# Optimization experiments

Hardware: AMD Instinct MI355X
Metric: run time of the kernel (lower is better)

## Reference

```python
import jax, jax.numpy as jnp
import numpy as np

K = 16  # knn_k
LN_EPS = 1e-5


def _layernorm(x, g, b):
    mu = jnp.mean(x, axis=-1, keepdims=True)
    var = jnp.var(x, axis=-1, keepdims=True)
    return (x - mu) * jax.lax.rsqrt(var + LN_EPS) * g + b


def _mlp_block(x, W1, b1, g, be, W2, b2):
    # Linear -> LayerNorm -> GELU -> Linear (MLPBlock)
    h = x @ W1 + b1
    h = jax.nn.gelu(_layernorm(h, g, be))
    return h @ W2 + b2


def _knn(v):
    # v: [N,3] -> indices of K nearest neighbors [N,K] (self included, as in knn search)
    sq = jnp.sum(v * v, axis=-1)                       # [N]
    d = sq[:, None] + sq[None, :] - 2.0 * (v @ v.T)    # [N,N] squared dists
    return jax.lax.top_k(-d, K)[1]                     # [N,K]


def setup_inputs() -> dict:
    key = jax.random.key(0)
    ks = jax.random.split(key, 8)
    B, N, C_IN, C_OUT, HID = 2, 8192, 32, 64, 128
    E_IN = C_IN + C_IN + 3  # 67
    s = 0.02
    return {
        "vertices": jax.random.normal(ks[0], (B, N, 3), jnp.float32),
        "features": jax.random.normal(ks[1], (B, N, C_IN), jnp.float32),
        "W1": jax.random.normal(ks[2], (E_IN, HID), jnp.float32) * s,
        "b1": jnp.zeros((HID,), jnp.float32),
        "g1": jnp.ones((HID,), jnp.float32),
        "be1": jnp.zeros((HID,), jnp.float32),
        "W2": jax.random.normal(ks[3], (HID, C_OUT), jnp.float32) * s,
        "b2": jnp.zeros((C_OUT,), jnp.float32),
        "Wo1": jax.random.normal(ks[4], (C_OUT, HID), jnp.float32) * s,
        "bo1": jnp.zeros((HID,), jnp.float32),
        "go": jnp.ones((HID,), jnp.float32),
        "beo": jnp.zeros((HID,), jnp.float32),
        "Wo2": jax.random.normal(ks[5], (HID, C_OUT), jnp.float32) * s,
        "bo2": jnp.zeros((C_OUT,), jnp.float32),
    }


def reference(vertices, features, W1, b1, g1, be1, W2, b2,
              Wo1, bo1, go, beo, Wo2, bo2):
    # out_point_feature_type == 'same': output points == input points
    idx = jax.vmap(_knn)(vertices)                                   # [B,N,K]
    gather = jax.vmap(lambda a, i: jnp.take(a, i, axis=0))
    neigh_feat = gather(features, idx)                               # [B,N,K,C]
    neigh_vert = gather(vertices, idx)                               # [B,N,K,3]
    self_feat = jnp.broadcast_to(features[:, :, None, :], neigh_feat.shape)
    rel_pos = neigh_vert - vertices[:, :, None, :]                   # [B,N,K,3]
    edge = jnp.concatenate([neigh_feat, self_feat, rel_pos], axis=-1)  # [B,N,K,2C+3]
    edge = _mlp_block(edge, W1, b1, g1, be1, W2, b2)                 # [B,N,K,C_out]
    out = jnp.mean(edge, axis=2)                                     # 'mean' reduction over K neighbors
    out = _mlp_block(out, Wo1, bo1, go, beo, Wo2, bo2)               # [B,N,C_out]
    return out
```

## Files before the change

### kernel.cpp

```cpp
#include <hip/hip_runtime.h>
#include <hip/hip_bf16.h>
#include <math.h>

#define BATCH 2
#define NPTS  8192
#define CIN   32
#define HID   128
#define COUT  64
#define EIN   67
#define KNN   16

#define TILE  1024
#define CAP   128
#define KMARGIN 1e-3f

typedef unsigned short u16;
typedef unsigned long long u64;
typedef __attribute__((ext_vector_type(8))) short bf16x8;
typedef __attribute__((ext_vector_type(4))) float f32x4;

#if defined(__has_builtin)
#if __has_builtin(__builtin_amdgcn_rcpf)
#define USE_RCPF 1
#endif
#endif

__device__ __forceinline__ u16 f2b(float f) {
    unsigned u = __float_as_uint(f);
    return (u16)((u + 0x7FFFu + ((u >> 16) & 1u)) >> 16);
}
__device__ __forceinline__ unsigned pk2(float a, float b) {
    return (unsigned)f2b(a) | ((unsigned)f2b(b) << 16);
}
__device__ __forceinline__ float gelu_t(float x) {
    float u = 1.5957691216057308f * (x + 0.044715f * x * x * x);
    float ex = __expf(u);
#ifdef USE_RCPF
    return x * ex * __builtin_amdgcn_rcpf(ex + 1.0f);
#else
    return x * ex / (ex + 1.0f);
#endif
}

__global__ void prep_kernel(const float* __restrict__ verts, float4* __restrict__ pv) {
    int i = blockIdx.x * blockDim.x + threadIdx.x;
    if (i >= BATCH * NPTS) return;
    float x = verts[3 * i], y = verts[3 * i + 1], z = verts[3 * i + 2];
    float sq = __fadd_rn(__fadd_rn(__fmul_rn(x, x), __fmul_rn(y, y)), __fmul_rn(z, z));
    pv[i] = make_float4(x, y, z, sq);
}

__global__ __launch_bounds__(256, 4) void knn7_kernel(const float4* __restrict__ pv,
                                                      int* __restrict__ nbr_out_rows) {
    __shared__ float4 minv4[4][64];
    __shared__ float  bufD[4][4][CAP];
    __shared__ int    bufJ[4][4][CAP];

    const int tid = threadIdx.x, lane = tid & 63, wv = tid >> 6;
    const int pt0 = (blockIdx.x * 4 + wv) * 4;
    const int b = pt0 >> 13, i0 = pt0 & (NPTS - 1);
    const float4* P = pv + (size_t)b * NPTS;

    float4 sp[4];
    float ax[4], ay[4], az[4];
#pragma unroll
    for (int p = 0; p < 4; ++p) {
        sp[p] = P[i0 + p];
        ax[p] = -2.0f * sp[p].x; ay[p] = -2.0f * sp[p].y; az[p] = -2.0f * sp[p].z;
    }

    float mn[4] = {INFINITY, INFINITY, INFINITY, INFINITY};
    for (int t = 0; t < 16; ++t) {
        float4 c0 = P[t * 256 + lane];
        float4 c1 = P[t * 256 + 64 + lane];
        float4 c2 = P[t * 256 + 128 + lane];
        float4 c3 = P[t * 256 + 192 + lane];
#pragma unroll
        for (int p = 0; p < 4; ++p) {
            float f0 = __fmaf_rn(ax[p], c0.x, __fmaf_rn(ay[p], c0.y, __fmaf_rn(az[p], c0.z, c0.w)));
            float f1 = __fmaf_rn(ax[p], c1.x, __fmaf_rn(ay[p], c1.y, __fmaf_rn(az[p], c1.z, c1.w)));
            float f2 = __fmaf_rn(ax[p], c2.x, __fmaf_rn(ay[p], c2.y, __fmaf_rn(az[p], c2.z, c2.w)));
            float f3 = __fmaf_rn(ax[p], c3.x, __fmaf_rn(ay[p], c3.y, __fmaf_rn(az[p], c3.z, c3.w)));
            mn[p] = fminf(fminf(fminf(mn[p], f0), fminf(f1, f2)), f3);
        }
    }

    minv4[wv][lane] = make_float4(mn[0], mn[1], mn[2], mn[3]);
    int rk[4] = {0, 0, 0, 0};
    for (int mm = 0; mm < 64; ++mm) {
        float4 v = minv4[wv][mm];
        rk[0] += (v.x < mn[0]) || (v.x == mn[0] && mm < lane);
        rk[1] += (v.y < mn[1]) || (v.y == mn[1] && mm < lane);
        rk[2] += (v.z < mn[2]) || (v.z == mn[2] && mm < lane);
        rk[3] += (v.w < mn[3]) || (v.w == mn[3] && mm < lane);
    }
    float tau[4];
#pragma unroll
    for (int p = 0; p < 4; ++p) {
        u64 bal = __ballot(rk[p] == 15);
        int srcl = __ffsll(bal) - 1;
        tau[p] = __shfl(mn[p], srcl, 64) + KMARGIN;
    }

    int base[4] = {0, 0, 0, 0};
    for (int t = 0; t < 32; ++t) {
        float4 c[4];
#pragma unroll
        for (int k = 0; k < 4; ++k) c[k] = P[t * 256 + k * 64 + lane];
        bool pr[4][4];
        bool anyl = false;
#pragma unroll
        for (int k = 0; k < 4; ++k)
#pragma unroll
            for (int p = 0; p < 4; ++p) {
                float f = __fmaf_rn(ax[p], c[k].x,
                          __fmaf_rn(ay[p], c[k].y,
                          __fmaf_rn(az[p], c[k].z, c[k].w)));
                pr[k][p] = (f <= tau[p]);
                anyl |= pr[k][p];
            }
        if (__ballot(anyl) == 0ull) continue;
#pragma unroll
        for (int k = 0; k < 4; ++k) {
            u64 anyk = __ballot(pr[k][0] | pr[k][1] | pr[k][2] | pr[k][3]);
            if (anyk == 0ull) continue;
            int j = t * 256 + k * 64 + lane;
#pragma unroll
            for (int p = 0; p < 4; ++p) {
                u64 mk = __ballot(pr[k][p]);
                if (mk != 0ull) {
                    if (pr[k][p]) {
                        int pos = base[p] + (int)__popcll(mk & ((1ull << lane) - 1ull));
                        if (pos < CAP) bufJ[wv][p][pos] = j;
                    }
                    base[p] += (int)__popcll(mk);
                }
            }
        }
    }

#pragma unroll
    for (int p = 0; p < 4; ++p) {
        int ns = base[p]; ns = (ns > CAP) ? CAP : ns;
        float dloc[2]; int jloc[2];
#pragma unroll
        for (int slot = 0; slot < 2; ++slot) {
            int sidx = slot * 64 + lane;
            bool act = sidx < ns;
            int js = act ? bufJ[wv][p][sidx] : 0;
            float4 cc = P[js];
            float dot = __fmul_rn(sp[p].x, cc.x);
            dot = __fmaf_rn(sp[p].y, cc.y, dot);
            dot = __fmaf_rn(sp[p].z, cc.z, dot);
            float d = __fsub_rn(__fadd_rn(sp[p].w, cc.w), __fmul_rn(2.0f, dot));
            if (act) bufD[wv][p][sidx] = d;
            dloc[slot] = d; jloc[slot] = js;
        }
        int r0 = 0, r1 = 0;
        for (int mm = 0; mm < ns; ++mm) {
            float dm = bufD[wv][p][mm]; int jm = bufJ[wv][p][mm];
            r0 += (dm < dloc[0]) || (dm == dloc[0] && jm < jloc[0]);
            r1 += (dm < dloc[1]) || (dm == dloc[1] && jm < jloc[1]);
        }
        if (lane < ns && r0 < KNN)
            nbr_out_rows[(size_t)(pt0 + p) * 64 + r0] = jloc[0];
        if (64 + lane < ns && r1 < KNN)
            nbr_out_rows[(size_t)(pt0 + p) * 64 + r1] = jloc[1];
    }
}

__global__ __launch_bounds__(256) void knn_kernel(const float* __restrict__ verts,
                                                  int* nbr_out_rows) {
    __shared__ float4 tilebuf[TILE];
    __shared__ float  bufD[4][CAP];
    __shared__ int    bufJ[4][CAP];

    const int tid = threadIdx.x, lane = tid & 63, wv = tid >> 6;
    const int pt = blockIdx.x * 4 + wv;
    const int b = pt >> 13, i = pt & (NPTS - 1);
    const float* vb = verts + (size_t)b * NPTS * 3;

    const float xi = vb[3 * i], yi = vb[3 * i + 1], zi = vb[3 * i + 2];
    const float sqi = __fadd_rn(__fadd_rn(__fmul_rn(xi, xi), __fmul_rn(yi, yi)),
                                __fmul_rn(zi, zi));

    float m_d = INFINITY;
    for (int t = 0; t < NPTS / TILE; ++t) {
        __syncthreads();
        for (int s = 0; s < TILE / 256; ++s) {
            int p = t * TILE + s * 256 + tid;
            float px = vb[3 * p], py = vb[3 * p + 1], pz = vb[3 * p + 2];
            float sq = __fadd_rn(__fadd_rn(__fmul_rn(px, px), __fmul_rn(py, py)),
                                 __fmul_rn(pz, pz));
            tilebuf[s * 256 + tid] = make_float4(px, py, pz, sq);
        }
        __syncthreads();
        for (int it = 0; it < TILE / 64; ++it) {
            float4 c = tilebuf[it * 64 + lane];
            float dot = __fmul_rn(xi, c.x);
            dot = __fmaf_rn(yi, c.y, dot);
            dot = __fmaf_rn(zi, c.z, dot);
            float d = __fsub_rn(__fadd_rn(sqi, c.w), __fmul_rn(2.0f, dot));
            m_d = fminf(m_d, d);
        }
    }
    __shared__ float minv[4][64];
    minv[wv][lane] = m_d;
    __syncthreads();
    int rnk = 0;
    for (int mm = 0; mm < 64; ++mm) {
        float vm = minv[wv][mm];
        rnk += (vm < m_d) || (vm == m_d && mm < lane);
    }
    u64 bal = __ballot(rnk == 15);
    float tau = __shfl(m_d, __ffsll(bal) - 1, 64);

    int base = 0;
    for (int t = 0; t < NPTS / TILE; ++t) {
        __syncthreads();
        for (int s = 0; s < TILE / 256; ++s) {
            int p = t * TILE + s * 256 + tid;
            float px = vb[3 * p], py = vb[3 * p + 1], pz = vb[3 * p + 2];
            float sq = __fadd_rn(__fadd_rn(__fmul_rn(px, px), __fmul_rn(py, py)),
                                 __fmul_rn(pz, pz));
            tilebuf[s * 256 + tid] = make_float4(px, py, pz, sq);
        }
        __syncthreads();
        for (int it = 0; it < TILE / 64; ++it) {
            int jl = it * 64 + lane;
            float4 c = tilebuf[jl];
            float dot = __fmul_rn(xi, c.x);
            dot = __fmaf_rn(yi, c.y, dot);
            dot = __fmaf_rn(zi, c.z, dot);
            float d = __fsub_rn(__fadd_rn(sqi, c.w), __fmul_rn(2.0f, dot));
            bool pred = (d <= tau);
            u64 mask = __ballot(pred);
            if (pred) {
                int pos = base + (int)__popcll(mask & ((1ull << lane) - 1ull));
                if (pos < CAP) { bufD[wv][pos] = d; bufJ[wv][pos] = t * TILE + jl; }
            }
            base += (int)__popcll(mask);
        }
    }
    int ns = (base > CAP) ? CAP : base;
    __syncthreads();
#pragma unroll
    for (int slot = 0; slot < 2; ++slot) {
        int sidx = slot * 64 + lane;
        if (sidx < ns) {
            float ds = bufD[wv][sidx];
            int   js = bufJ[wv][sidx];
            int rank = 0;
            for (int mm = 0; mm < ns; ++mm) {
                float dm = bufD[wv][mm];
                int   jm = bufJ[wv][mm];
                rank += (dm < ds) || (dm == ds && jm < js);
            }
            if (rank < KNN) nbr_out_rows[(size_t)pt * 64 + rank] = js;
        }
    }
}

__global__ __launch_bounds__(256, 2) void edge4_kernel(
    const float* __restrict__ verts, const float* __restrict__ feats,
    const float* __restrict__ W1, const float* __restrict__ b1,
    const float* __restrict__ g1, const float* __restrict__ be1,
    const float* __restrict__ W2, const float* __restrict__ b2,
    const float* __restrict__ Wo1, const float* __restrict__ bo1,
    const float* __restrict__ go_, const float* __restrict__ beo,
    const float* __restrict__ Wo2, const float* __restrict__ bo2,
    float* out)
{
    __shared__ u16 EPw[4][4][64][8];
    __shared__ u16 W1F[3][8][64][8];
    __shared__ float b1s[HID], g1s[HID], be1s[HID];
    __shared__ float b2s[COUT];
    __shared__ float meansh[16][68];

    const int tid  = threadIdx.x;
    const int lane = tid & 63, wv = tid >> 6;
    const int quad = lane >> 4, n16 = lane & 15;

    for (int s = tid; s < 3 * 8 * 64; s += 256) {
        int kt = s >> 9, nt = (s >> 6) & 7, ln = s & 63;
        int q = ln >> 4, nn = ln & 15;
        int col = nt * 16 + nn;
        union { bf16x8 v; unsigned u[4]; } pk;
#pragma unroll
        for (int jj = 0; jj < 4; ++jj) {
            int k0 = kt * 32 + q * 8 + jj * 2;
            float a  = (k0     < EIN) ? W1[(size_t)k0 * HID + col]       : 0.0f;
            float bq = (k0 + 1 < EIN) ? W1[(size_t)(k0 + 1) * HID + col] : 0.0f;
            pk.u[jj] = pk2(a, bq);
        }
        *(bf16x8*)&W1F[kt][nt][ln][0] = pk.v;
    }
    if (tid < HID) { b1s[tid] = b1[tid]; g1s[tid] = g1[tid]; be1s[tid] = be1[tid]; }
    if (tid < COUT) b2s[tid] = b2[tid];

    bf16x8 w2r[4][4];
#pragma unroll
    for (int kt2 = 0; kt2 < 4; ++kt2)
#pragma unroll
        for (int nt2 = 0; nt2 < 4; ++nt2) {
            union { bf16x8 v; unsigned u[4]; } pk;
#pragma unroll
            for (int jj = 0; jj < 4; ++jj) {
                int k0 = kt2 * 32 + quad * 8 + jj * 2;
                int o = nt2 * 16 + n16;
                pk.u[jj] = pk2(W2[(size_t)k0 * COUT + o],
                               W2[(size_t)(k0 + 1) * COUT + o]);
            }
            w2r[kt2][nt2] = pk.v;
        }
    __syncthreads();

    const int ptb = blockIdx.x * 16;
    const int bb  = ptb >> 13;
    const float* fb  = feats + (size_t)bb * NPTS * CIN;
    const float* vbk = verts + (size_t)bb * NPTS * 3;
    const int ptw = ptb + wv * 4;
    const int ipw = ptw & (NPTS - 1);

    float b1v[8], g1v[8], bev[8];
#pragma unroll
    for (int nt = 0; nt < 8; ++nt) {
        b1v[nt] = b1s[nt * 16 + n16];
        g1v[nt] = g1s[nt * 16 + n16];
        bev[nt] = be1s[nt * 16 + n16];
    }

    const int k16 = lane & 15;
    const int qq  = lane >> 4;

    int jnv[4];
#pragma unroll
    for (int pp = 0; pp < 4; ++pp)
        jnv[pp] = ((const int*)out)[(size_t)(ptw + pp) * 64 + k16];

#pragma unroll
    for (int pp = 0; pp < 4; ++pp) {
        const int jn  = jnv[pp];
        const int ipn = ipw + pp;

        {
            const float* nsrc = fb + (size_t)jn * CIN + qq * 8;
            float4 nA = *(const float4*)nsrc, nB = *(const float4*)(nsrc + 4);
            const float* ssrc = fb + (size_t)ipn * CIN + qq * 8;
            float4 sA = *(const float4*)ssrc, sB = *(const float4*)(ssrc + 4);

            union { bf16x8 v; unsigned u[4]; } e0, e1, e2;
            e0.u[0] = pk2(nA.x, nA.y); e0.u[1] = pk2(nA.z, nA.w);
            e0.u[2] = pk2(nB.x, nB.y); e0.u[3] = pk2(nB.z, nB.w);
            e1.u[0] = pk2(sA.x, sA.y); e1.u[1] = pk2(sA.z, sA.w);
            e1.u[2] = pk2(sB.x, sB.y); e1.u[3] = pk2(sB.z, sB.w);
            e2.u[0] = e2.u[1] = e2.u[2] = e2.u[3] = 0u;
            if (qq == 0) {
                float rx = vbk[3 * jn]     - vbk[3 * ipn];
                float ry = vbk[3 * jn + 1] - vbk[3 * ipn + 1];
                float rz = vbk[3 * jn + 2] - vbk[3 * ipn + 2];
                e2.u[0] = pk2(rx, ry); e2.u[1] = pk2(rz, 0.0f);
            }
            *(bf16x8*)&EPw[wv][0][lane][0] = e0.v;
            *(bf16x8*)&EPw[wv][1][lane][0] = e1.v;
            *(bf16x8*)&EPw[wv][2][lane][0] = e2.v;
        }

        f32x4 acc[8];
#pragma unroll
        for (int nt = 0; nt < 8; ++nt) acc[nt] = (f32x4){0.f, 0.f, 0.f, 0.f};
#pragma unroll
        for (int kt = 0; kt < 3; ++kt) {
            bf16x8 a = *(bf16x8*)&EPw[wv][kt][lane][0];
#pragma unroll
            for (int nt = 0; nt < 8; ++nt) {
                bf16x8 bfr = *(bf16x8*)&W1F[kt][nt][lane][0];
                acc[nt] = __builtin_amdgcn_mfma_f32_16x16x32_bf16(a, bfr, acc[nt], 0, 0, 0);
            }
        }

        float s1[4] = {0,0,0,0}, s2[4] = {0,0,0,0};
#pragma unroll
        for (int nt = 0; nt < 8; ++nt)
#pragma unroll
            for (int r = 0; r < 4; ++r) {
                float x = acc[nt][r] + b1v[nt];
                s1[r] += x; s2[r] += x * x;
            }
#pragma unroll
        for (int r = 0; r < 4; ++r) {
#pragma unroll
            for (int off = 1; off < 16; off <<= 1) {
                s1[r] += __shfl_xor(s1[r], off, 64);
                s2[r] += __shfl_xor(s2[r], off, 64);
            }
        }
        float mu[4], rs[4];
#pragma unroll
        for (int r = 0; r < 4; ++r) {
            mu[r] = s1[r] * (1.0f / HID);
            float var = s2[r] * (1.0f / HID) - mu[r] * mu[r];
            rs[r] = rsqrtf(var + 1e-5f);
        }

#pragma unroll
        for (int nt = 0; nt < 8; ++nt) {
            int kt2 = nt >> 1;
            int q2  = (nt * 2 + (n16 >> 3)) & 3;
            int jj  = n16 & 7;
#pragma unroll
            for (int r = 0; r < 4; ++r) {
                float x  = acc[nt][r] + b1v[nt];
                float xn = (x - mu[r]) * rs[r] * g1v[nt] + bev[nt];
                EPw[wv][kt2][quad * 4 + r + 16 * q2][jj] = (u16)f2b(gelu_t(xn));
            }
        }

        f32x4 acc2[4];
#pragma unroll
        for (int nt2 = 0; nt2 < 4; ++nt2) acc2[nt2] = (f32x4){0.f, 0.f, 0.f, 0.f};
#pragma unroll
        for (int kt2 = 0; kt2 < 4; ++kt2) {
            bf16x8 a2 = *(bf16x8*)&EPw[wv][kt2][lane][0];
#pragma unroll
            for (int nt2 = 0; nt2 < 4; ++nt2)
                acc2[nt2] = __builtin_amdgcn_mfma_f32_16x16x32_bf16(a2, w2r[kt2][nt2], acc2[nt2], 0, 0, 0);
        }

#pragma unroll
        for (int nt2 = 0; nt2 < 4; ++nt2) {
            float cs = acc2[nt2][0] + acc2[nt2][1] + acc2[nt2][2] + acc2[nt2][3];
            cs += __shfl_xor(cs, 16, 64);
            cs += __shfl_xor(cs, 32, 64);
            if (quad == 0) {
                int o = nt2 * 16 + n16;
                meansh[wv * 4 + pp][o] = cs * (1.0f / KNN) + b2s[o];
            }
        }
    }

    __syncthreads();

    for (int s = tid; s < 2 * 8 * 64; s += 256) {
        int kt = s >> 9, nt = (s >> 6) & 7, ln = s & 63;
        int q = ln >> 4, nn = ln & 15;
        int col = nt * 16 + nn;
        union { bf16x8 v; unsigned u[4]; } pk;
#pragma unroll
        for (int jj = 0; jj < 4; ++jj) {
            int k0 = kt * 32 + q * 8 + jj * 2;
            pk.u[jj] = pk2(Wo1[(size_t)k0 * HID + col],
                           Wo1[(size_t)(k0 + 1) * HID + col]);
        }
        *(bf16x8*)&W1F[kt][nt][ln][0] = pk.v;
    }
    if (tid < HID) { b1s[tid] = bo1[tid]; g1s[tid] = go_[tid]; be1s[tid] = beo[tid]; }
    if (tid < COUT) b2s[tid] = bo2[tid];
#pragma unroll
    for (int kt2 = 0; kt2 < 4; ++kt2)
#pragma unroll
        for (int nt2 = 0; nt2 < 4; ++nt2) {
            union { bf16x8 v; unsigned u[4]; } pk;
#pragma unroll
            for (int jj = 0; jj < 4; ++jj) {
                int k0 = kt2 * 32 + quad * 8 + jj * 2;
                int o = nt2 * 16 + n16;
                pk.u[jj] = pk2(Wo2[(size_t)k0 * COUT + o],
                               Wo2[(size_t)(k0 + 1) * COUT + o]);
            }
            w2r[kt2][nt2] = pk.v;
        }
    __syncthreads();

    if (wv == 0) {
        bf16x8 af[2];
#pragma unroll
        for (int kt = 0; kt < 2; ++kt) {
            const float* mrow = &meansh[n16][kt * 32 + quad * 8];
            float4 A = *(const float4*)mrow, B4 = *(const float4*)(mrow + 4);
            union { bf16x8 v; unsigned u[4]; } pk;
            pk.u[0] = pk2(A.x, A.y); pk.u[1] = pk2(A.z, A.w);
            pk.u[2] = pk2(B4.x, B4.y); pk.u[3] = pk2(B4.z, B4.w);
            af[kt] = pk.v;
        }

        f32x4 acc[8];
#pragma unroll
        for (int nt = 0; nt < 8; ++nt) acc[nt] = (f32x4){0.f, 0.f, 0.f, 0.f};
#pragma unroll
        for (int kt = 0; kt < 2; ++kt)
#pragma unroll
            for (int nt = 0; nt < 8; ++nt) {
                bf16x8 bfr = *(bf16x8*)&W1F[kt][nt][lane][0];
                acc[nt] = __builtin_amdgcn_mfma_f32_16x16x32_bf16(af[kt], bfr, acc[nt], 0, 0, 0);
            }

        float pb1[8], pg1[8], pbe[8];
#pragma unroll
        for (int nt = 0; nt < 8; ++nt) {
            pb1[nt] = b1s[nt * 16 + n16];
            pg1[nt] = g1s[nt * 16 + n16];
            pbe[nt] = be1s[nt * 16 + n16];
        }
        float s1[4] = {0,0,0,0}, s2[4] = {0,0,0,0};
#pragma unroll
        for (int nt = 0; nt < 8; ++nt)
#pragma unroll
            for (int r = 0; r < 4; ++r) {
                float x = acc[nt][r] + pb1[nt];
                s1[r] += x; s2[r] += x * x;
            }
#pragma unroll
        for (int r = 0; r < 4; ++r) {
#pragma unroll
            for (int off = 1; off < 16; off <<= 1) {
                s1[r] += __shfl_xor(s1[r], off, 64);
                s2[r] += __shfl_xor(s2[r], off, 64);
            }
        }
#pragma unroll
        for (int nt = 0; nt < 8; ++nt) {
            int kt2 = nt >> 1;
            int q2  = (nt * 2 + (n16 >> 3)) & 3;
            int jj  = n16 & 7;
#pragma unroll
            for (int r = 0; r < 4; ++r) {
                float mu = s1[r] * (1.0f / HID);
                float var = s2[r] * (1.0f / HID) - mu * mu;
                float rs = rsqrtf(var + 1e-5f);
                float x  = acc[nt][r] + pb1[nt];
                float xn = (x - mu) * rs * pg1[nt] + pbe[nt];
                EPw[0][kt2][quad * 4 + r + 16 * q2][jj] = (u16)f2b(gelu_t(xn));
            }
        }

        f32x4 acc2[4];
#pragma unroll
        for (int nt2 = 0; nt2 < 4; ++nt2) acc2[nt2] = (f32x4){0.f, 0.f, 0.f, 0.f};
#pragma unroll
        for (int kt2 = 0; kt2 < 4; ++kt2) {
            bf16x8 a2 = *(bf16x8*)&EPw[0][kt2][lane][0];
#pragma unroll
            for (int nt2 = 0; nt2 < 4; ++nt2)
                acc2[nt2] = __builtin_amdgcn_mfma_f32_16x16x32_bf16(a2, w2r[kt2][nt2], acc2[nt2], 0, 0, 0);
        }

#pragma unroll
        for (int nt2 = 0; nt2 < 4; ++nt2) {
            int o = nt2 * 16 + n16;
#pragma unroll
            for (int r = 0; r < 4; ++r)
                meansh[quad * 4 + r][o] = acc2[nt2][r] + b2s[o];
        }
    }
    __syncthreads();

    {
        int p = tid >> 4, c = (tid & 15) * 4;
        float4 v = *(const float4*)&meansh[p][c];
        *(float4*)&out[(size_t)(ptb + p) * 64 + c] = v;
    }
}

extern "C" void kernel_launch(void* const* d_in, const int* in_sizes, int n_in,
                              void* d_out, int out_size, void* d_ws, size_t ws_size,
                              hipStream_t stream) {
    const float* verts = (const float*)d_in[0];
    const float* feats = (const float*)d_in[1];
    const float* W1  = (const float*)d_in[2];
    const float* b1  = (const float*)d_in[3];
    const float* g1  = (const float*)d_in[4];
    const float* be1 = (const float*)d_in[5];
    const float* W2  = (const float*)d_in[6];
    const float* b2  = (const float*)d_in[7];
    const float* Wo1 = (const float*)d_in[8];
    const float* bo1 = (const float*)d_in[9];
    const float* go_ = (const float*)d_in[10];
    const float* beo = (const float*)d_in[11];
    const float* Wo2 = (const float*)d_in[12];
    const float* bo2 = (const float*)d_in[13];
    float* out = (float*)d_out;

    (void)in_sizes; (void)n_in; (void)out_size;

    const size_t pv_bytes = (size_t)BATCH * NPTS * sizeof(float4);
    if (ws_size >= pv_bytes) {
        float4* pv = (float4*)d_ws;
        prep_kernel<<<(BATCH * NPTS + 255) / 256, 256, 0, stream>>>(verts, pv);
        knn7_kernel<<<(BATCH * NPTS) / 16, 256, 0, stream>>>(pv, (int*)out);
    } else {
        knn_kernel<<<(BATCH * NPTS) / 4, 256, 0, stream>>>(verts, (int*)out);
    }
    edge4_kernel<<<(BATCH * NPTS) / 16, 256, 0, stream>>>(
        verts, feats, W1, b1, g1, be1, W2, b2,
        Wo1, bo1, go_, beo, Wo2, bo2, out);
}
```

Baseline: 211.9 us.

## Halve queries per wave in KNN and use bitonic shuffle to find threshold

Each wave now handles 2 query points instead of 4, doubling the grid and raising the launch-bounds occupancy hint to 8 blocks. The LDS-based 64-way rank count for the 16th-smallest lane minimum is replaced by an in-register bitonic sort across the wave using xor shuffles. This aims to expose more parallelism and cut the serial shared-memory loop, at the cost of reading the candidate point array twice as many times overall.

```diff
diff --git a/kernel.cpp b/kernel.cpp
--- a/kernel.cpp
+++ b/kernel.cpp
@@ -42,6 +42,21 @@
 #endif
 }
 
+__device__ __forceinline__ float rank16_of_64(float v, int lane) {
+#pragma unroll
+    for (int k = 2; k <= 64; k <<= 1) {
+#pragma unroll
+        for (int j = k >> 1; j > 0; j >>= 1) {
+            float o = __shfl_xor(v, j, 64);
+            bool lower = (lane & j) == 0;
+            bool asc   = (lane & k) == 0;
+            float mn = fminf(v, o), mx = fmaxf(v, o);
+            v = (lower == asc) ? mn : mx;
+        }
+    }
+    return __shfl(v, 15, 64);
+}
+
 __global__ void prep_kernel(const float* __restrict__ verts, float4* __restrict__ pv) {
     int i = blockIdx.x * blockDim.x + threadIdx.x;
     if (i >= BATCH * NPTS) return;
@@ -50,33 +65,32 @@
     pv[i] = make_float4(x, y, z, sq);
 }
 
-__global__ __launch_bounds__(256, 4) void knn7_kernel(const float4* __restrict__ pv,
+__global__ __launch_bounds__(256, 8) void knn9_kernel(const float4* __restrict__ pv,
                                                       int* __restrict__ nbr_out_rows) {
-    __shared__ float4 minv4[4][64];
-    __shared__ float  bufD[4][4][CAP];
-    __shared__ int    bufJ[4][4][CAP];
+    __shared__ float  bufD[4][2][CAP];
+    __shared__ int    bufJ[4][2][CAP];
 
     const int tid = threadIdx.x, lane = tid & 63, wv = tid >> 6;
-    const int pt0 = (blockIdx.x * 4 + wv) * 4;
+    const int pt0 = (blockIdx.x * 4 + wv) * 2;
     const int b = pt0 >> 13, i0 = pt0 & (NPTS - 1);
     const float4* P = pv + (size_t)b * NPTS;
 
-    float4 sp[4];
-    float ax[4], ay[4], az[4];
-#pragma unroll
-    for (int p = 0; p < 4; ++p) {
+    float4 sp[2];
+    float ax[2], ay[2], az[2];
+#pragma unroll
+    for (int p = 0; p < 2; ++p) {
         sp[p] = P[i0 + p];
         ax[p] = -2.0f * sp[p].x; ay[p] = -2.0f * sp[p].y; az[p] = -2.0f * sp[p].z;
     }
 
-    float mn[4] = {INFINITY, INFINITY, INFINITY, INFINITY};
+    float mn[2] = {INFINITY, INFINITY};
     for (int t = 0; t < 16; ++t) {
         float4 c0 = P[t * 256 + lane];
         float4 c1 = P[t * 256 + 64 + lane];
         float4 c2 = P[t * 256 + 128 + lane];
         float4 c3 = P[t * 256 + 192 + lane];
 #pragma unroll
-        for (int p = 0; p < 4; ++p) {
+        for (int p = 0; p < 2; ++p) {
             float f0 = __fmaf_rn(ax[p], c0.x, __fmaf_rn(ay[p], c0.y, __fmaf_rn(az[p], c0.z, c0.w)));
             float f1 = __fmaf_rn(ax[p], c1.x, __fmaf_rn(ay[p], c1.y, __fmaf_rn(az[p], c1.z, c1.w)));
             float f2 = __fmaf_rn(ax[p], c2.x, __fmaf_rn(ay[p], c2.y, __fmaf_rn(az[p], c2.z, c2.w)));
@@ -85,34 +99,22 @@
         }
     }
 
-    minv4[wv][lane] = make_float4(mn[0], mn[1], mn[2], mn[3]);
-    int rk[4] = {0, 0, 0, 0};
-    for (int mm = 0; mm < 64; ++mm) {
-        float4 v = minv4[wv][mm];
-        rk[0] += (v.x < mn[0]) || (v.x == mn[0] && mm < lane);
-        rk[1] += (v.y < mn[1]) || (v.y == mn[1] && mm < lane);
-        rk[2] += (v.z < mn[2]) || (v.z == mn[2] && mm < lane);
-        rk[3] += (v.w < mn[3]) || (v.w == mn[3] && mm < lane);
-    }
-    float tau[4];
-#pragma unroll
-    for (int p = 0; p < 4; ++p) {
-        u64 bal = __ballot(rk[p] == 15);
-        int srcl = __ffsll(bal) - 1;
-        tau[p] = __shfl(mn[p], srcl, 64) + KMARGIN;
-    }
-
-    int base[4] = {0, 0, 0, 0};
+    float tau[2];
+#pragma unroll
+    for (int p = 0; p < 2; ++p)
+        tau[p] = rank16_of_64(mn[p], lane) + KMARGIN;
+
+    int base[2] = {0, 0};
     for (int t = 0; t < 32; ++t) {
         float4 c[4];
 #pragma unroll
         for (int k = 0; k < 4; ++k) c[k] = P[t * 256 + k * 64 + lane];
-        bool pr[4][4];
+        bool pr[4][2];
         bool anyl = false;
 #pragma unroll
         for (int k = 0; k < 4; ++k)
 #pragma unroll
-            for (int p = 0; p < 4; ++p) {
+            for (int p = 0; p < 2; ++p) {
                 float f = __fmaf_rn(ax[p], c[k].x,
                           __fmaf_rn(ay[p], c[k].y,
                           __fmaf_rn(az[p], c[k].z, c[k].w)));
@@ -122,11 +124,11 @@
         if (__ballot(anyl) == 0ull) continue;
 #pragma unroll
         for (int k = 0; k < 4; ++k) {
-            u64 anyk = __ballot(pr[k][0] | pr[k][1] | pr[k][2] | pr[k][3]);
+            u64 anyk = __ballot(pr[k][0] | pr[k][1]);
             if (anyk == 0ull) continue;
             int j = t * 256 + k * 64 + lane;
 #pragma unroll
-            for (int p = 0; p < 4; ++p) {
+            for (int p = 0; p < 2; ++p) {
                 u64 mk = __ballot(pr[k][p]);
                 if (mk != 0ull) {
                     if (pr[k][p]) {
@@ -140,7 +142,7 @@
     }
 
 #pragma unroll
-    for (int p = 0; p < 4; ++p) {
+    for (int p = 0; p < 2; ++p) {
         int ns = base[p]; ns = (ns > CAP) ? CAP : ns;
         float dloc[2]; int jloc[2];
 #pragma unroll
@@ -587,7 +589,7 @@
     if (ws_size >= pv_bytes) {
         float4* pv = (float4*)d_ws;
         prep_kernel<<<(BATCH * NPTS + 255) / 256, 256, 0, stream>>>(verts, pv);
-        knn7_kernel<<<(BATCH * NPTS) / 16, 256, 0, stream>>>(pv, (int*)out);
+        knn9_kernel<<<(BATCH * NPTS) / 8, 256, 0, stream>>>(pv, (int*)out);
     } else {
         knn_kernel<<<(BATCH * NPTS) / 4, 256, 0, stream>>>(verts, (int*)out);
     }
```

New measurement: 208.1 us. About the same (-1.8%).
